# Optimization experiments

Measured on AMD Instinct MI355X. Metric: run time of the kernel, lower is better.

## Reference

```python
import jax, jax.numpy as jnp
import numpy as np

NUM_GRAPHS = 1024
NODES_PER_GRAPH = 256
NUM_NODES = NUM_GRAPHS * NODES_PER_GRAPH  # 262144
EMBED_DIM = 300
EPS = 1e-12


def setup_inputs() -> dict:
    key = jax.random.key(0)
    tensor = jax.random.normal(key, (NUM_NODES, EMBED_DIM), dtype=jnp.float32)
    # per-graph node counts; equal-sized graphs summing exactly to NUM_NODES
    batch_list = jnp.full((NUM_GRAPHS,), NODES_PER_GRAPH, dtype=jnp.int64)
    return {"tensor": tensor, "batch_list": batch_list}


def reference(tensor, batch_list):
    # tensor: [N, D] node features; batch_list: [B] nodes per graph
    B = batch_list.shape[0]
    N = tensor.shape[0]
    # segment id per node (repeat_interleave of graph index)
    seg = jnp.repeat(jnp.arange(B), batch_list, total_repeat_length=N)  # [N]
    tmax = jax.ops.segment_max(tensor, seg, num_segments=B)  # [B, D]
    tmin = jax.ops.segment_min(tensor, seg, num_segments=B)  # [B, D]
    mid = (tmax + tmin) * 0.5
    ldv = (tmax - tmin) * 0.5
    # gather per-graph stats back to nodes (repeat)
    mid_n = mid[seg]                       # [N, D]
    ldv_n = jnp.maximum(ldv[seg], EPS)     # clamp: ldv[ldv<=1e-12]=1e-12
    return (tensor - mid_n) / ldv_n
```

## Files before the change

### kernel.cpp

```cpp
#include <hip/hip_runtime.h>
#include <float.h>


#define NUM_GRAPHS 1024
#define NODES      256
#define DIMS       300
#define CHUNK      64
#define NCHUNK     5
#define EPS        1e-12f

typedef float v4f __attribute__((ext_vector_type(4)));

__device__ __forceinline__ float4 f4min(float4 a, float4 b) {
    return make_float4(fminf(a.x, b.x), fminf(a.y, b.y),
                       fminf(a.z, b.z), fminf(a.w, b.w));
}
__device__ __forceinline__ float4 f4max(float4 a, float4 b) {
    return make_float4(fmaxf(a.x, b.x), fmaxf(a.y, b.y),
                       fmaxf(a.z, b.z), fmaxf(a.w, b.w));
}

__global__ __launch_bounds__(256, 4) void cube_norm_kernel(
    const float* __restrict__ in, float* __restrict__ out)
{
    const int chunk = blockIdx.x;
    const int g     = blockIdx.y;
    const int tid   = threadIdx.x;
    const int x     = tid & 15;
    const int y     = tid >> 4;
    const int wv    = tid >> 6;
    const int lane  = tid & 63;
    const int d0    = chunk * CHUNK + x * 4;
    const bool active = d0 < DIMS;

    const size_t graph_base = (size_t)g * NODES * DIMS;
    const float* gin  = in  + graph_base;
    float*       gout = out + graph_base;

    float4 vals[16];
    float4 vmin = make_float4( FLT_MAX,  FLT_MAX,  FLT_MAX,  FLT_MAX);
    float4 vmax = make_float4(-FLT_MAX, -FLT_MAX, -FLT_MAX, -FLT_MAX);

    if (active) {
#pragma unroll
        for (int i = 0; i < 16; ++i) {
            const int node = i * 16 + y;
            float4 v = *(const float4*)(gin + (size_t)node * DIMS + d0);
            asm volatile("" : "+v"(v.x), "+v"(v.y), "+v"(v.z), "+v"(v.w));
            vals[i] = v;
            vmin = f4min(vmin, v);
            vmax = f4max(vmax, v);
        }
    }

#pragma unroll
    for (int s = 16; s <= 32; s += s) {
        vmin.x = fminf(vmin.x, __shfl_xor(vmin.x, s));
        vmin.y = fminf(vmin.y, __shfl_xor(vmin.y, s));
        vmin.z = fminf(vmin.z, __shfl_xor(vmin.z, s));
        vmin.w = fminf(vmin.w, __shfl_xor(vmin.w, s));
        vmax.x = fmaxf(vmax.x, __shfl_xor(vmax.x, s));
        vmax.y = fmaxf(vmax.y, __shfl_xor(vmax.y, s));
        vmax.z = fmaxf(vmax.z, __shfl_xor(vmax.z, s));
        vmax.w = fmaxf(vmax.w, __shfl_xor(vmax.w, s));
    }

    __shared__ float4 smn[4][16];
    __shared__ float4 smx[4][16];
    if (lane < 16) { smn[wv][lane] = vmin; smx[wv][lane] = vmax; }
    __syncthreads();

    const float4 mn = f4min(f4min(smn[0][x], smn[1][x]),
                            f4min(smn[2][x], smn[3][x]));
    const float4 mx = f4max(f4max(smx[0][x], smx[1][x]),
                            f4max(smx[2][x], smx[3][x]));

    float4 mid, inv;
    mid.x = (mx.x + mn.x) * 0.5f;
    mid.y = (mx.y + mn.y) * 0.5f;
    mid.z = (mx.z + mn.z) * 0.5f;
    mid.w = (mx.w + mn.w) * 0.5f;
    inv.x = 1.0f / fmaxf((mx.x - mn.x) * 0.5f, EPS);
    inv.y = 1.0f / fmaxf((mx.y - mn.y) * 0.5f, EPS);
    inv.z = 1.0f / fmaxf((mx.z - mn.z) * 0.5f, EPS);
    inv.w = 1.0f / fmaxf((mx.w - mn.w) * 0.5f, EPS);

    if (active) {
#pragma unroll
        for (int i = 0; i < 16; ++i) {
            const int node = i * 16 + y;
            const float4 v = vals[i];
            v4f o = { (v.x - mid.x) * inv.x,
                      (v.y - mid.y) * inv.y,
                      (v.z - mid.z) * inv.z,
                      (v.w - mid.w) * inv.w };
            __builtin_nontemporal_store(
                o, (v4f*)(gout + (size_t)node * DIMS + d0));
        }
    }
}

extern "C" void kernel_launch(void* const* d_in, const int* in_sizes, int n_in,
                              void* d_out, int out_size, void* d_ws, size_t ws_size,
                              hipStream_t stream) {
    const float* tensor = (const float*)d_in[0];
    float* out = (float*)d_out;

    dim3 grid(NCHUNK, NUM_GRAPHS);
    dim3 block(256);
    cube_norm_kernel<<<grid, block, 0, stream>>>(tensor, out);
}
```

Measured before the change: 603.6 us.

## Process one graph per block and re-read inputs instead of caching in registers

Each block now handles a whole graph: 640 threads laid out as 80 float4 columns by 8 row groups. Each thread walks 32 rows per pass instead of holding 16 float4 values in registers. The second pass re-reads the input from memory, counting on L2/MALL hits since each graph is about 300 KB. This gives fully contiguous rows per block and lower register pressure, but adds a second read of the input, and 5 of the 80 columns in each row group sit idle.

```diff
diff --git a/kernel.cpp b/kernel.cpp
--- a/kernel.cpp
+++ b/kernel.cpp
@@ -5,8 +5,11 @@
 #define NUM_GRAPHS 1024
 #define NODES      256
 #define DIMS       300
-#define CHUNK      64
-#define NCHUNK     5
+#define F4ROW      75
+#define XL         80
+#define RPI        8
+#define NIT        32
+#define UNROLL     4
 #define EPS        1e-12f
 
 typedef float v4f __attribute__((ext_vector_type(4)));
@@ -20,60 +23,52 @@
                        fmaxf(a.z, b.z), fmaxf(a.w, b.w));
 }
 
-__global__ __launch_bounds__(256, 4) void cube_norm_kernel(
+__global__ __launch_bounds__(640) void cube_norm_kernel(
     const float* __restrict__ in, float* __restrict__ out)
 {
-    const int chunk = blockIdx.x;
-    const int g     = blockIdx.y;
-    const int tid   = threadIdx.x;
-    const int x     = tid & 15;
-    const int y     = tid >> 4;
-    const int wv    = tid >> 6;
-    const int lane  = tid & 63;
-    const int d0    = chunk * CHUNK + x * 4;
-    const bool active = d0 < DIMS;
+    const int g   = blockIdx.x;
+    const int tid = threadIdx.x;
+    const int x   = tid % XL;
+    const int y   = tid / XL;
+    const bool active = x < F4ROW;
 
     const size_t graph_base = (size_t)g * NODES * DIMS;
     const float* gin  = in  + graph_base;
     float*       gout = out + graph_base;
 
-    float4 vals[16];
     float4 vmin = make_float4( FLT_MAX,  FLT_MAX,  FLT_MAX,  FLT_MAX);
     float4 vmax = make_float4(-FLT_MAX, -FLT_MAX, -FLT_MAX, -FLT_MAX);
 
     if (active) {
+        const float* p = gin + (size_t)y * DIMS + 4 * x;
+        for (int it = 0; it < NIT; it += UNROLL) {
+            float4 v[UNROLL];
 #pragma unroll
-        for (int i = 0; i < 16; ++i) {
-            const int node = i * 16 + y;
-            float4 v = *(const float4*)(gin + (size_t)node * DIMS + d0);
-            asm volatile("" : "+v"(v.x), "+v"(v.y), "+v"(v.z), "+v"(v.w));
-            vals[i] = v;
-            vmin = f4min(vmin, v);
-            vmax = f4max(vmax, v);
+            for (int u = 0; u < UNROLL; ++u) {
+                const int row = (it + u) * RPI;
+                v[u] = *(const float4*)(p + (size_t)row * DIMS);
+            }
+#pragma unroll
+            for (int u = 0; u < UNROLL; ++u) {
+                vmin = f4min(vmin, v[u]);
+                vmax = f4max(vmax, v[u]);
+            }
         }
     }
 
-#pragma unroll
-    for (int s = 16; s <= 32; s += s) {
-        vmin.x = fminf(vmin.x, __shfl_xor(vmin.x, s));
-        vmin.y = fminf(vmin.y, __shfl_xor(vmin.y, s));
-        vmin.z = fminf(vmin.z, __shfl_xor(vmin.z, s));
-        vmin.w = fminf(vmin.w, __shfl_xor(vmin.w, s));
-        vmax.x = fmaxf(vmax.x, __shfl_xor(vmax.x, s));
-        vmax.y = fmaxf(vmax.y, __shfl_xor(vmax.y, s));
-        vmax.z = fmaxf(vmax.z, __shfl_xor(vmax.z, s));
-        vmax.w = fmaxf(vmax.w, __shfl_xor(vmax.w, s));
-    }
-
-    __shared__ float4 smn[4][16];
-    __shared__ float4 smx[4][16];
-    if (lane < 16) { smn[wv][lane] = vmin; smx[wv][lane] = vmax; }
+    __shared__ float4 smn[RPI][XL];
+    __shared__ float4 smx[RPI][XL];
+    smn[y][x] = vmin;
+    smx[y][x] = vmax;
     __syncthreads();
 
-    const float4 mn = f4min(f4min(smn[0][x], smn[1][x]),
-                            f4min(smn[2][x], smn[3][x]));
-    const float4 mx = f4max(f4max(smx[0][x], smx[1][x]),
-                            f4max(smx[2][x], smx[3][x]));
+    float4 mn = smn[0][x];
+    float4 mx = smx[0][x];
+#pragma unroll
+    for (int j = 1; j < RPI; ++j) {
+        mn = f4min(mn, smn[j][x]);
+        mx = f4max(mx, smx[j][x]);
+    }
 
     float4 mid, inv;
     mid.x = (mx.x + mn.x) * 0.5f;
@@ -86,16 +81,24 @@
     inv.w = 1.0f / fmaxf((mx.w - mn.w) * 0.5f, EPS);
 
     if (active) {
+        const float* p = gin  + (size_t)y * DIMS + 4 * x;
+        float*       q = gout + (size_t)y * DIMS + 4 * x;
+        for (int it = 0; it < NIT; it += UNROLL) {
+            float4 v[UNROLL];
 #pragma unroll
-        for (int i = 0; i < 16; ++i) {
-            const int node = i * 16 + y;
-            const float4 v = vals[i];
-            v4f o = { (v.x - mid.x) * inv.x,
-                      (v.y - mid.y) * inv.y,
-                      (v.z - mid.z) * inv.z,
-                      (v.w - mid.w) * inv.w };
-            __builtin_nontemporal_store(
-                o, (v4f*)(gout + (size_t)node * DIMS + d0));
+            for (int u = 0; u < UNROLL; ++u) {
+                const int row = (it + u) * RPI;
+                v[u] = *(const float4*)(p + (size_t)row * DIMS);
+            }
+#pragma unroll
+            for (int u = 0; u < UNROLL; ++u) {
+                const int row = (it + u) * RPI;
+                v4f o = { (v[u].x - mid.x) * inv.x,
+                          (v[u].y - mid.y) * inv.y,
+                          (v[u].z - mid.z) * inv.z,
+                          (v[u].w - mid.w) * inv.w };
+                __builtin_nontemporal_store(o, (v4f*)(q + (size_t)row * DIMS));
+            }
         }
     }
 }
@@ -106,7 +109,7 @@
     const float* tensor = (const float*)d_in[0];
     float* out = (float*)d_out;
 
-    dim3 grid(NCHUNK, NUM_GRAPHS);
-    dim3 block(256);
+    dim3 grid(NUM_GRAPHS);
+    dim3 block(XL * RPI);
     cube_norm_kernel<<<grid, block, 0, stream>>>(tensor, out);
 }
```

New measurement: 546.7 us. -9.4%, faster.
